# Kernel tuning notes

Hardware: AMD Instinct MI355X
Metric: run time of the kernel (lower is better)

The kernel has to match this reference:

```python
import jax, jax.numpy as jnp
import numpy as np

D_MODEL, D_STATE, D_CONV, EXPAND, HEADDIM, NGROUPS, CHUNK = 1024, 64, 4, 2, 64, 1, 64
D_INNER = EXPAND * D_MODEL          # 2048
NHEADS = D_INNER // HEADDIM         # 32
CONV_DIM = D_INNER + 2 * NGROUPS * D_STATE  # 2176
D_IN_PROJ = 2 * D_INNER + 2 * NGROUPS * D_STATE + NHEADS  # 4256
EPS = 1e-5


def segsum(x):
    """x: (..., T) -> (..., T, T) with out[i,j]=sum_{j<k<=i} x[k], -inf above diag."""
    T = x.shape[-1]
    i = jnp.arange(T)[:, None]
    j = jnp.arange(T)[None, :]
    xr = jnp.where(i > j, x[..., :, None], 0.0)   # keep x[...,i] at (i,j) when i>j
    s = jnp.cumsum(xr, axis=-2)
    return jnp.where(i >= j, s, -jnp.inf)


def setup_inputs() -> dict:
    key = jax.random.key(0)
    ks = jax.random.split(key, 10)
    B, L = 4, 4096
    u = jax.random.normal(ks[0], (B, L, D_MODEL), dtype=jnp.float32)
    in_proj_w = jax.random.normal(ks[1], (D_IN_PROJ, D_MODEL), dtype=jnp.float32) * (D_MODEL ** -0.5)
    conv_w = jax.random.normal(ks[2], (CONV_DIM, D_CONV), dtype=jnp.float32) * (D_CONV ** -0.5)
    conv_b = jax.random.normal(ks[3], (CONV_DIM,), dtype=jnp.float32) * 0.02
    init_states = jax.random.normal(ks[4], (NHEADS, HEADDIM, D_STATE), dtype=jnp.float32) * 0.02
    # dt_bias = inv softplus of dt sampled log-uniform in [1e-3, 1e-1]
    dt = jnp.exp(jax.random.uniform(ks[5], (NHEADS,)) * (np.log(0.1) - np.log(0.001)) + np.log(0.001))
    dt = jnp.clip(dt, 1e-4, None)
    dt_bias = dt + jnp.log(-jnp.expm1(-dt))
    A_log = jnp.log(jax.random.uniform(ks[6], (NHEADS,), minval=1.0, maxval=16.0))
    D = jnp.ones((NHEADS,), dtype=jnp.float32)
    norm_w = jnp.ones((D_INNER,), dtype=jnp.float32)
    out_proj_w = jax.random.normal(ks[7], (D_MODEL, D_INNER), dtype=jnp.float32) * (D_INNER ** -0.5)
    return {"u": u, "in_proj_w": in_proj_w, "conv_w": conv_w, "conv_b": conv_b,
            "init_states": init_states, "dt_bias": dt_bias, "A_log": A_log, "D": D,
            "norm_w": norm_w, "out_proj_w": out_proj_w}


def _forward(u, in_proj_w, conv_w, conv_b, init_states, dt_bias, A_log, D, norm_w, out_proj_w):
    b, L, _ = u.shape
    zxbcdt = jnp.einsum('bld,ed->ble', u, in_proj_w)
    z = zxbcdt[..., :D_INNER]
    xBC = zxbcdt[..., D_INNER:D_INNER + CONV_DIM]
    dt = jax.nn.softplus(zxbcdt[..., D_INNER + CONV_DIM:] + dt_bias)  # (b,L,h)
    # causal depthwise conv1d (padding=K-1, truncated to L) + SiLU
    xp = jnp.pad(xBC, ((0, 0), (D_CONV - 1, 0), (0, 0)))
    xBC = sum(xp[:, k:k + L, :] * conv_w[:, k] for k in range(D_CONV)) + conv_b
    xBC = jax.nn.silu(xBC)
    x = xBC[..., :D_INNER].reshape(b, L, NHEADS, HEADDIM)
    Bm = xBC[..., D_INNER:D_INNER + NGROUPS * D_STATE].reshape(b, L, NGROUPS, D_STATE)
    Cm = xBC[..., D_INNER + NGROUPS * D_STATE:].reshape(b, L, NGROUPS, D_STATE)
    A = -jnp.exp(A_log)  # (h,)
    # broadcast groups to heads (torch einsum broadcasts size-1 group dim)
    Bm = jnp.repeat(Bm, NHEADS // NGROUPS, axis=2)
    Cm = jnp.repeat(Cm, NHEADS // NGROUPS, axis=2)
    X = x * dt[..., None]          # (b,L,h,p)
    Adt = A * dt                   # (b,L,h)
    c = L // CHUNK
    Xc = X.reshape(b, c, CHUNK, NHEADS, HEADDIM)
    Bc = Bm.reshape(b, c, CHUNK, NHEADS, D_STATE)
    Cc = Cm.reshape(b, c, CHUNK, NHEADS, D_STATE)
    Ac = Adt.reshape(b, c, CHUNK, NHEADS).transpose(0, 3, 1, 2)  # (b,h,c,l)
    A_cumsum = jnp.cumsum(Ac, axis=-1)
    Lmat = jnp.exp(segsum(Ac))  # (b,h,c,l,l)
    Y_diag = jnp.einsum('bclhn,bcshn,bhcls,bcshp->bclhp', Cc, Bc, Lmat, Xc)
    decay_states = jnp.exp(A_cumsum[..., -1:] - A_cumsum)  # (b,h,c,l)
    states = jnp.einsum('bclhn,bhcl,bclhp->bchpn', Bc, decay_states, Xc)
    init = jnp.broadcast_to(init_states, (b,) + init_states.shape)[:, None]  # (b,1,h,p,n)
    states = jnp.concatenate([init, states], axis=1)  # (b,c+1,h,p,n)
    decay_chunk = jnp.exp(segsum(jnp.pad(A_cumsum[..., -1], ((0, 0), (0, 0), (1, 0)))))
    new_states = jnp.einsum('bhzc,bchpn->bzhpn', decay_chunk, states)
    states = new_states[:, :-1]
    state_decay_out = jnp.exp(A_cumsum)
    Y_off = jnp.einsum('bclhn,bchpn,bhcl->bclhp', Cc, states, state_decay_out)
    Y = (Y_diag + Y_off).reshape(b, L, NHEADS, HEADDIM) + x * D[:, None]
    y = Y.reshape(b, L, D_INNER)
    # gated RMSNorm (gate before norm)
    y = y * jax.nn.silu(z)
    y = y * jax.lax.rsqrt(jnp.mean(y * y, axis=-1, keepdims=True) + EPS) * norm_w
    return jnp.einsum('bld,ed->ble', y, out_proj_w)


def reference(u, in_proj_w, conv_w, conv_b, init_states, dt_bias, A_log, D, norm_w, out_proj_w):
    return _forward(u, in_proj_w, conv_w, conv_b, init_states, dt_bias, A_log, D, norm_w, out_proj_w)
```

## Files before the change

kernel.cpp:

```cpp
#include <hip/hip_runtime.h>
#include <math.h>

#define BATCH  4
#define LSEQ   4096
#define DMODEL 1024
#define DINNER 2048
#define NH     32
#define HD     64
#define DSTATE 64
#define CONVD  2176
#define NPROJ  4352
#define ZROW   4224
#define NCHUNK 64

typedef __attribute__((ext_vector_type(8))) short bf16x8;
typedef __attribute__((ext_vector_type(4))) float f32x4;

__device__ __forceinline__ float sigm(float x){ return 1.f/(1.f+expf(-x)); }

__device__ __forceinline__ unsigned short f2bf(float x){
    unsigned u = __float_as_uint(x);
    unsigned r = (u + 0x7fffu + ((u>>16)&1u)) >> 16;
    return (unsigned short)r;
}
__device__ __forceinline__ float bf2f(unsigned short h){
    return __uint_as_float(((unsigned)h)<<16);
}

__device__ __forceinline__ void gl2lds16(const unsigned short* g, short* l){
    __builtin_amdgcn_global_load_lds(
        (const __attribute__((address_space(1))) unsigned int*)g,
        (__attribute__((address_space(3))) unsigned int*)l, 16, 0, 0);
}

__global__ __launch_bounds__(256)
void f32_to_bf16(const float* __restrict__ in, unsigned short* __restrict__ o, size_t n)
{
    size_t i = ((size_t)blockIdx.x*256 + threadIdx.x)*8;
    if (i >= n) return;
    float4 a = *(const float4*)(in + i);
    float4 b = *(const float4*)(in + i + 4);
    uint4 v;
    v.x = (unsigned)f2bf(a.x) | ((unsigned)f2bf(a.y)<<16);
    v.y = (unsigned)f2bf(a.z) | ((unsigned)f2bf(a.w)<<16);
    v.z = (unsigned)f2bf(b.x) | ((unsigned)f2bf(b.y)<<16);
    v.w = (unsigned)f2bf(b.z) | ((unsigned)f2bf(b.w)<<16);
    *(uint4*)(o + i) = v;
}

template<int EPI>
__global__ __launch_bounds__(256)
void gemm_mfma(const unsigned short* __restrict__ A,
               const unsigned short* __restrict__ B,
               int K, int lda, int ldc, int ntiles, int Mrows,
               float* __restrict__ Cf,
               unsigned short* __restrict__ zxbc,
               float* __restrict__ dtout,
               const float* __restrict__ dt_bias,
               unsigned short* __restrict__ halo)
{
    __shared__ short As[128*32];
    __shared__ short Bs[128*32];
    const int tid  = threadIdx.x;
    const int wave = tid >> 6;
    const int lane = tid & 63;

    const int GM  = 16;
    const int pid = blockIdx.x;
    const int gsz = GM * ntiles;
    const int grp = pid / gsz;
    const int rem = pid - grp*gsz;
    const int bm  = (grp*GM + (rem & (GM-1))) * 128;
    const int bn  = (rem / GM) * 128;

    const int wr = (wave >> 1) * 64;
    const int wc = (wave & 1) * 64;
    const int quad = lane >> 4;
    const int l15  = lane & 15;

    f32x4 acc[4][4];
    #pragma unroll
    for (int i=0;i<4;i++)
        #pragma unroll
        for (int j=0;j<4;j++)
            acc[i][j] = (f32x4){0.f,0.f,0.f,0.f};

    const int srow = (lane >> 2);
    const int skc  = (lane & 3) * 8;

    for (int k0 = 0; k0 < K; k0 += 32){
        #pragma unroll
        for (int s=0; s<4; s++){
            int t = wave*4 + s;
            int r = (t & 7)*16 + srow;
            if (t < 8)
                gl2lds16(A + (size_t)(bm + r)*lda + k0 + skc, &As[(t & 7)*512]);
            else
                gl2lds16(B + (size_t)(bn + r)*K + k0 + skc, &Bs[(t & 7)*512]);
        }
        __syncthreads();
        bf16x8 af[4], bg[4];
        #pragma unroll
        for (int i=0;i<4;i++)
            af[i] = *(const bf16x8*)&As[(wr + i*16 + l15)*32 + quad*8];
        #pragma unroll
        for (int j=0;j<4;j++)
            bg[j] = *(const bf16x8*)&Bs[(wc + j*16 + l15)*32 + quad*8];
        #pragma unroll
        for (int i=0;i<4;i++)
            #pragma unroll
            for (int j=0;j<4;j++)
                acc[i][j] = __builtin_amdgcn_mfma_f32_16x16x32_bf16(af[i], bg[j], acc[i][j], 0,0,0);
        __syncthreads();
    }

    if (EPI == 0){
        #pragma unroll
        for (int i=0;i<4;i++)
            #pragma unroll
            for (int j=0;j<4;j++){
                int col = bn + wc + j*16 + l15;
                #pragma unroll
                for (int r=0;r<4;r++){
                    int row = bm + wr + i*16 + quad*4 + r;
                    Cf[(size_t)row*ldc + col] = acc[i][j][r];
                }
            }
    } else {
        if (bn < DINNER){
            #pragma unroll
            for (int i=0;i<4;i++)
                #pragma unroll
                for (int r=0;r<4;r++){
                    int row = bm + wr + i*16 + quad*4 + r;
                    #pragma unroll
                    for (int j=0;j<4;j++){
                        int col = bn + wc + j*16 + l15;
                        zxbc[(size_t)row*ZROW + col] = f2bf(acc[i][j][r]);
                    }
                }
        } else if (bn < DINNER + CONVD){
            #pragma unroll
            for (int i=0;i<4;i++)
                #pragma unroll
                for (int r=0;r<4;r++){
                    int row = bm + wr + i*16 + quad*4 + r;
                    int rel = row & 63;
                    int seg = (row >> 6) + 1;
                    #pragma unroll
                    for (int j=0;j<4;j++){
                        int col = bn + wc + j*16 + l15;
                        unsigned short v = f2bf(acc[i][j][r]);
                        zxbc[(size_t)row*ZROW + col] = v;
                        if (rel >= 61 && seg*64 < Mrows)
                            halo[((size_t)(seg*3 + (rel-61)))*CONVD + (col - DINNER)] = v;
                    }
                }
        } else if (wc == 0){
            #pragma unroll
            for (int j=0;j<2;j++){
                int h = j*16 + l15;
                #pragma unroll
                for (int i=0;i<4;i++)
                    #pragma unroll
                    for (int r=0;r<4;r++){
                        int row = bm + wr + i*16 + quad*4 + r;
                        float t = acc[i][j][r] + dt_bias[h];
                        dtout[(size_t)row*NH + h] = (t > 20.f) ? t : log1pf(expf(t));
                    }
            }
        }
    }
}

__global__ __launch_bounds__(256)
void conv_inplace(unsigned short* __restrict__ zxbc,
                  const unsigned short* __restrict__ halo,
                  const float* __restrict__ conv_w, const float* __restrict__ conv_b)
{
    int c = blockIdx.x*256 + threadIdx.x;
    if (c >= CONVD) return;
    int seg = blockIdx.y;
    const float w0=conv_w[c*4+0], w1=conv_w[c*4+1], w2=conv_w[c*4+2], w3=conv_w[c*4+3];
    const float bias = conv_b[c];
    float x0=0.f, x1=0.f, x2=0.f;
    if ((seg & 63) != 0){
        const unsigned short* hp = halo + (size_t)(seg*3)*CONVD + c;
        x0 = bf2f(hp[0]); x1 = bf2f(hp[CONVD]); x2 = bf2f(hp[2*CONVD]);
    }
    unsigned short* p = zxbc + (size_t)(seg*64)*ZROW + DINNER + c;
    for (int i=0;i<64;i++){
        float x3 = bf2f(*p);
        float v = fmaf(w0,x0,fmaf(w1,x1,fmaf(w2,x2,fmaf(w3,x3,bias))));
        *p = f2bf(v * sigm(v));
        x0=x1; x1=x2; x2=x3; p += ZROW;
    }
}

__global__ __launch_bounds__(256)
void states_intra(const unsigned short* __restrict__ zxbc,
                  const float* __restrict__ dtbuf,
                  const float* __restrict__ A_log,
                  unsigned short* __restrict__ locst,
                  float* __restrict__ acsbuf,
                  float* __restrict__ csumbuf)
{
    const int h = blockIdx.x, c = blockIdx.y;
    __shared__ unsigned short XT[64*72];
    __shared__ unsigned short BT[64*72];
    __shared__ float dt_sh[64], acs_sh[64], w_sh[64];
    const int tid = threadIdx.x;
    const size_t row0 = (size_t)(c*64)*ZROW;

    if (tid < 64) dt_sh[tid] = dtbuf[(size_t)(c*64+tid)*NH + h];
    __syncthreads();
    if (tid == 0){
        float Ah = -expf(A_log[h]); float s = 0.f;
        for (int l=0;l<64;l++){ s = fmaf(Ah, dt_sh[l], s); acs_sh[l] = s; }
    }
    __syncthreads();
    const float a63 = acs_sh[63];
    if (tid < 64){
        float a = acs_sh[tid];
        acsbuf[((size_t)c*NH + h)*64 + tid] = a;
        w_sh[tid] = expf(a63 - a) * dt_sh[tid];
    }
    if (tid == 0) csumbuf[(size_t)c*NH + h] = a63;
    __syncthreads();

    {
        const int l  = tid >> 2;
        const int f4 = tid & 3;
        const unsigned short* xr = zxbc + row0 + (size_t)l*ZROW;
        const float w = w_sh[l];
        #pragma unroll
        for (int q=0;q<4;q++){
            int col = f4*4 + q*16;
            uint2 xv = *(const uint2*)(xr + DINNER + h*HD + col);
            uint2 bv = *(const uint2*)(xr + DINNER + DINNER + col);
            XT[(col+0)*72 + l] = (unsigned short)(xv.x & 0xffff);
            XT[(col+1)*72 + l] = (unsigned short)(xv.x >> 16);
            XT[(col+2)*72 + l] = (unsigned short)(xv.y & 0xffff);
            XT[(col+3)*72 + l] = (unsigned short)(xv.y >> 16);
            BT[(col+0)*72 + l] = f2bf(bf2f((unsigned short)(bv.x & 0xffff))*w);
            BT[(col+1)*72 + l] = f2bf(bf2f((unsigned short)(bv.x >> 16))*w);
            BT[(col+2)*72 + l] = f2bf(bf2f((unsigned short)(bv.y & 0xffff))*w);
            BT[(col+3)*72 + l] = f2bf(bf2f((unsigned short)(bv.y >> 16))*w);
        }
    }
    __syncthreads();

    const int wave = tid >> 6, lane = tid & 63;
    const int quad = lane >> 4, l15 = lane & 15;
    f32x4 acc[4];
    #pragma unroll
    for (int j=0;j<4;j++) acc[j] = (f32x4){0.f,0.f,0.f,0.f};
    #pragma unroll
    for (int ks=0;ks<2;ks++){
        bf16x8 af = *(const bf16x8*)&XT[(wave*16 + l15)*72 + ks*32 + quad*8];
        #pragma unroll
        for (int j=0;j<4;j++){
            bf16x8 bf = *(const bf16x8*)&BT[(j*16 + l15)*72 + ks*32 + quad*8];
            acc[j] = __builtin_amdgcn_mfma_f32_16x16x32_bf16(af, bf, acc[j], 0,0,0);
        }
    }
    const size_t sbase = ((size_t)c*NH + h)*4096;
    #pragma unroll
    for (int j=0;j<4;j++)
        #pragma unroll
        for (int r=0;r<4;r++){
            int p = wave*16 + quad*4 + r;
            int n = j*16 + l15;
            locst[sbase + (size_t)p*64 + n] = f2bf(acc[j][r]);
        }
}

__global__ __launch_bounds__(256)
void chunk_scan(unsigned short* __restrict__ states,
                const float* __restrict__ csumbuf,
                const float* __restrict__ init_states)
{
    const int h = blockIdx.x, half = blockIdx.y, b = blockIdx.z;
    __shared__ float cs_sh[64];
    const int tid = threadIdx.x;
    if (tid < 64) cs_sh[tid] = csumbuf[(size_t)(b*64 + tid)*NH + h];
    __syncthreads();
    const int e0 = half*2048 + tid*8;
    float S[8];
    {
        const float4* ip = (const float4*)(init_states + (size_t)h*4096 + e0);
        float4 v0 = ip[0], v1 = ip[1];
        S[0]=v0.x; S[1]=v0.y; S[2]=v0.z; S[3]=v0.w;
        S[4]=v1.x; S[5]=v1.y; S[6]=v1.z; S[7]=v1.w;
    }
    for (int zg=0; zg<8; zg++){
        uint4 L[8];
        #pragma unroll
        for (int k=0;k<8;k++)
            L[k] = *(const uint4*)(states + ((size_t)(b*64 + zg*8+k)*NH + h)*4096 + e0);
        #pragma unroll
        for (int k=0;k<8;k++){
            int z = zg*8 + k;
            float dec = expf(cs_sh[z]);
            uint4 o;
            o.x = (unsigned)f2bf(S[0]) | ((unsigned)f2bf(S[1])<<16);
            o.y = (unsigned)f2bf(S[2]) | ((unsigned)f2bf(S[3])<<16);
            o.z = (unsigned)f2bf(S[4]) | ((unsigned)f2bf(S[5])<<16);
            o.w = (unsigned)f2bf(S[6]) | ((unsigned)f2bf(S[7])<<16);
            *(uint4*)(states + ((size_t)(b*64 + z)*NH + h)*4096 + e0) = o;
            unsigned a[4] = {L[k].x, L[k].y, L[k].z, L[k].w};
            #pragma unroll
            for (int q=0;q<4;q++){
                float lo = bf2f((unsigned short)(a[q]&0xffff));
                float hi = bf2f((unsigned short)(a[q]>>16));
                S[q*2+0] = fmaf(dec, S[q*2+0], lo);
                S[q*2+1] = fmaf(dec, S[q*2+1], hi);
            }
        }
    }
}

__global__ __launch_bounds__(256)
void y_fused(unsigned short* __restrict__ zxbc,
             const float* __restrict__ dtbuf,
             const unsigned short* __restrict__ entst,
             const float* __restrict__ acsbuf,
             const float* __restrict__ Dvec)
{
    const int h = blockIdx.x, c = blockIdx.y;
    __shared__ unsigned short Cr[64*72];
    __shared__ unsigned short Ce[64*72];
    __shared__ unsigned short Bm[64*72];
    __shared__ unsigned short XT[64*72];
    __shared__ unsigned short Sv[64*72];
    __shared__ float acs_sh[64], dt_sh[64], ea_sh[64];
    const int tid = threadIdx.x;
    const size_t row0 = (size_t)(c*64)*ZROW;
    const size_t sbase = ((size_t)c*NH + h)*4096;

    if (tid < 64){
        float a = acsbuf[((size_t)c*NH + h)*64 + tid];
        acs_sh[tid] = a;
        ea_sh[tid]  = expf(a);
        dt_sh[tid]  = dtbuf[(size_t)(c*64 + tid)*NH + h];
    }
    __syncthreads();

    {
        const int l  = tid >> 2;
        const int f4 = tid & 3;
        const unsigned short* xr = zxbc + row0 + (size_t)l*ZROW;
        const float el = ea_sh[l];
        #pragma unroll
        for (int q=0;q<4;q++){
            int col = f4*4 + q*16;
            uint2 cv = *(const uint2*)(xr + DINNER + DINNER + DSTATE + col);
            uint2 bv = *(const uint2*)(xr + DINNER + DINNER + col);
            uint2 xv = *(const uint2*)(xr + DINNER + h*HD + col);
            *(uint2*)&Cr[l*72 + col] = cv;
            *(uint2*)&Bm[l*72 + col] = bv;
            unsigned short* ce = &Ce[l*72 + col];
            ce[0] = f2bf(bf2f((unsigned short)(cv.x & 0xffff))*el);
            ce[1] = f2bf(bf2f((unsigned short)(cv.x >> 16))*el);
            ce[2] = f2bf(bf2f((unsigned short)(cv.y & 0xffff))*el);
            ce[3] = f2bf(bf2f((unsigned short)(cv.y >> 16))*el);
            XT[(col+0)*72 + l] = (unsigned short)(xv.x & 0xffff);
            XT[(col+1)*72 + l] = (unsigned short)(xv.x >> 16);
            XT[(col+2)*72 + l] = (unsigned short)(xv.y & 0xffff);
            XT[(col+3)*72 + l] = (unsigned short)(xv.y >> 16);
            *(uint2*)&Sv[l*72 + col] = *(const uint2*)(entst + sbase + (size_t)l*64 + col);
        }
    }
    __syncthreads();

    const int wave = tid >> 6, lane = tid & 63;
    const int quad = lane >> 4, l15 = lane & 15;

    f32x4 g[4];
    #pragma unroll
    for (int j=0;j<4;j++) g[j] = (f32x4){0.f,0.f,0.f,0.f};
    #pragma unroll
    for (int ks=0;ks<2;ks++){
        bf16x8 af = *(const bf16x8*)&Cr[(wave*16 + l15)*72 + ks*32 + quad*8];
        #pragma unroll
        for (int j=0;j<4;j++){
            bf16x8 bf = *(const bf16x8*)&Bm[(j*16 + l15)*72 + ks*32 + quad*8];
            g[j] = __builtin_amdgcn_mfma_f32_16x16x32_bf16(af, bf, g[j], 0,0,0);
        }
    }
    __syncthreads();

    const float Dh = Dvec[h];
    #pragma unroll
    for (int j=0;j<4;j++)
        #pragma unroll
        for (int r=0;r<4;r++){
            int l = wave*16 + quad*4 + r;
            int s = j*16 + l15;
            float v = (s <= l) ? g[j][r]*expf(acs_sh[l]-acs_sh[s])*dt_sh[s] : 0.f;
            if (s == l) v += Dh;
            Bm[l*72 + s] = f2bf(v);
        }
    __syncthreads();

    f32x4 y[4];
    #pragma unroll
    for (int j=0;j<4;j++) y[j] = (f32x4){0.f,0.f,0.f,0.f};
    #pragma unroll
    for (int ks=0;ks<2;ks++){
        bf16x8 a1 = *(const bf16x8*)&Bm[(wave*16 + l15)*72 + ks*32 + quad*8];
        bf16x8 a2 = *(const bf16x8*)&Ce[(wave*16 + l15)*72 + ks*32 + quad*8];
        #pragma unroll
        for (int j=0;j<4;j++){
            bf16x8 b1 = *(const bf16x8*)&XT[(j*16 + l15)*72 + ks*32 + quad*8];
            bf16x8 b2 = *(const bf16x8*)&Sv[(j*16 + l15)*72 + ks*32 + quad*8];
            y[j] = __builtin_amdgcn_mfma_f32_16x16x32_bf16(a1, b1, y[j], 0,0,0);
            y[j] = __builtin_amdgcn_mfma_f32_16x16x32_bf16(a2, b2, y[j], 0,0,0);
        }
    }

    #pragma unroll
    for (int j=0;j<4;j++)
        #pragma unroll
        for (int r=0;r<4;r++){
            int l = wave*16 + quad*4 + r;
            int p = j*16 + l15;
            zxbc[row0 + (size_t)l*ZROW + DINNER + h*HD + p] = f2bf(y[j][r]);
        }
}

__global__ __launch_bounds__(256)
void gate_norm(unsigned short* __restrict__ zxbc, const float* __restrict__ norm_w)
{
    const int m = blockIdx.x;
    const int tid = threadIdx.x;
    unsigned short* row = zxbc + (size_t)m*ZROW;
    uint4 zv = *(const uint4*)(row + tid*8);
    uint4 yv = *(const uint4*)(row + DINNER + tid*8);
    unsigned zz[4] = {zv.x, zv.y, zv.z, zv.w};
    unsigned yy[4] = {yv.x, yv.y, yv.z, yv.w};
    float g[8];
    float acc = 0.f;
    #pragma unroll
    for (int q=0;q<4;q++){
        float zl = bf2f((unsigned short)(zz[q]&0xffff));
        float zh = bf2f((unsigned short)(zz[q]>>16));
        float yl = bf2f((unsigned short)(yy[q]&0xffff));
        float yh = bf2f((unsigned short)(yy[q]>>16));
        g[q*2+0] = yl * zl * sigm(zl);
        g[q*2+1] = yh * zh * sigm(zh);
        acc += g[q*2]*g[q*2] + g[q*2+1]*g[q*2+1];
    }
    #pragma unroll
    for (int o=32;o>0;o>>=1) acc += __shfl_down(acc, o, 64);
    __shared__ float red[4];
    if ((tid & 63)==0) red[tid>>6] = acc;
    __syncthreads();
    float tot = red[0]+red[1]+red[2]+red[3];
    float scale = rsqrtf(tot * (1.f/2048.f) + 1e-5f);
    const float* nw = norm_w + tid*8;
    float4 w0 = *(const float4*)nw;
    float4 w1 = *(const float4*)(nw+4);
    float Wv[8] = {w0.x,w0.y,w0.z,w0.w,w1.x,w1.y,w1.z,w1.w};
    uint4 ov;
    unsigned ow[4];
    #pragma unroll
    for (int q=0;q<4;q++){
        unsigned short lo = f2bf(g[q*2+0]*scale*Wv[q*2+0]);
        unsigned short hi = f2bf(g[q*2+1]*scale*Wv[q*2+1]);
        ow[q] = (unsigned)lo | ((unsigned)hi<<16);
    }
    ov.x=ow[0]; ov.y=ow[1]; ov.z=ow[2]; ov.w=ow[3];
    *(uint4*)(row + tid*8) = ov;
}

extern "C" void kernel_launch(void* const* d_in, const int* in_sizes, int n_in,
                              void* d_out, int out_size, void* d_ws, size_t ws_size,
                              hipStream_t stream) {
    const float* u           = (const float*)d_in[0];
    const float* in_proj_w   = (const float*)d_in[1];
    const float* conv_w      = (const float*)d_in[2];
    const float* conv_b      = (const float*)d_in[3];
    const float* init_states = (const float*)d_in[4];
    const float* dt_bias     = (const float*)d_in[5];
    const float* A_log       = (const float*)d_in[6];
    const float* Dv          = (const float*)d_in[7];
    const float* norm_w      = (const float*)d_in[8];
    const float* out_proj_w  = (const float*)d_in[9];
    float* out = (float*)d_out;
    char* wsb = (char*)d_ws;

    const size_t BIG_BYTES = 226197504;
    const bool big = (ws_size >= BIG_BYTES);
    const int nb = big ? BATCH : 1;
    const size_t Mrows = (size_t)nb * LSEQ;

    size_t off = 0;
    unsigned short* zxbc    = (unsigned short*)(wsb + off); off += Mrows*ZROW*2;
    unsigned short* statesz = (unsigned short*)(wsb + off);
    unsigned short* ubf     = statesz;
    off += Mrows/64 * NH*HD*DSTATE*2;
    unsigned short* wibf    = (unsigned short*)(wsb + off); off += (size_t)NPROJ*DMODEL*2;
    unsigned short* woutbf  = (unsigned short*)(wsb + off); off += (size_t)DMODEL*DINNER*2;
    float*          dtbuf   = (float*)(wsb + off);   off += Mrows*NH*4;
    float*          acsbuf  = (float*)(wsb + off);   off += Mrows/64 * NH*64*4;
    float*          csumbuf = (float*)(wsb + off);   off += Mrows/64 * NH*4;
    unsigned short* halo    = (unsigned short*)(wsb + off); off += Mrows/64 * 3*CONVD*2;

    f32_to_bf16<<<dim3((4256*1024/8 + 255)/256), 256, 0, stream>>>(
        in_proj_w, wibf, (size_t)4256*1024);
    f32_to_bf16<<<dim3(1024*2048/8/256), 256, 0, stream>>>(
        out_proj_w, woutbf, (size_t)1024*2048);

    const int npass = big ? 1 : BATCH;
    for (int b=0; b<npass; b++){
        const float* ub   = u   + (size_t)b*LSEQ*DMODEL;
        float*       outb = out + (size_t)b*LSEQ*DMODEL;
        const int mt = (int)(Mrows/128);

        f32_to_bf16<<<dim3(Mrows*DMODEL/8/256), 256, 0, stream>>>(
            ub, ubf, Mrows*DMODEL);
        gemm_mfma<1><<<dim3((NPROJ/128) * mt), 256, 0, stream>>>(
            ubf, wibf, DMODEL, DMODEL, 0, NPROJ/128, (int)Mrows,
            nullptr, zxbc, dtbuf, dt_bias, halo);
        conv_inplace<<<dim3(9, (unsigned)(Mrows/64)), 256, 0, stream>>>(
            zxbc, halo, conv_w, conv_b);
        states_intra<<<dim3(NH, (unsigned)(Mrows/64)), 256, 0, stream>>>(
            zxbc, dtbuf, A_log, statesz, acsbuf, csumbuf);
        chunk_scan<<<dim3(NH, 2, nb), 256, 0, stream>>>(
            statesz, csumbuf, init_states);
        y_fused<<<dim3(NH, (unsigned)(Mrows/64)), 256, 0, stream>>>(
            zxbc, dtbuf, statesz, acsbuf, Dv);
        gate_norm<<<dim3((unsigned)Mrows), 256, 0, stream>>>(zxbc, norm_w);
        gemm_mfma<0><<<dim3((DMODEL/128) * mt), 256, 0, stream>>>(
            zxbc, woutbf, DINNER, ZROW, DMODEL, DMODEL/128, (int)Mrows,
            outb, nullptr, nullptr, nullptr, nullptr);
    }
}
```

Baseline: 646.0 us.

## Replace 128x128 GEMM with 256x256 multi-buffered pipelined MFMA kernel

Both projection GEMMs move to a new 512-thread kernel with 256x256 tiles. It keeps a 4-stage LDS ring buffer filled by direct global-to-LDS loads that are prefetched three k-steps ahead, and uses an XOR-swizzled LDS layout. MFMA bursts are split into two halves, each bracketed by s_setprio and explicit waitcnt/barrier control, and workgroups are remapped with an XCD-aware interleave. The aim is to hide memory latency and raise arithmetic intensity per tile. In exchange it uses far more LDS and registers (lower occupancy), and the 256-wide N tiles make the in-proj epilogue branch per 16-column sub-block.

```diff
diff --git a/kernel.cpp b/kernel.cpp
--- a/kernel.cpp
+++ b/kernel.cpp
@@ -33,6 +33,12 @@
         (__attribute__((address_space(3))) unsigned int*)l, 16, 0, 0);
 }
 
+__device__ __forceinline__ void wg_bar(){
+    asm volatile("" ::: "memory");
+    __builtin_amdgcn_s_barrier();
+    asm volatile("" ::: "memory");
+}
+
 __global__ __launch_bounds__(256)
 void f32_to_bf16(const float* __restrict__ in, unsigned short* __restrict__ o, size_t n)
 {
@@ -48,128 +54,147 @@
     *(uint4*)(o + i) = v;
 }
 
+__device__ __forceinline__ void stage_tile(const unsigned short* __restrict__ G,
+                                           int ld, int b0, int kt,
+                                           short* sl, int wid, int lane)
+{
+    const int r  = lane >> 2;
+    const int sc = (((lane & 3) ^ ((lane >> 3) & 3)) << 3);
+    #pragma unroll
+    for (int c=0;c<2;c++){
+        int row = wid*32 + c*16 + r;
+        gl2lds16(G + (size_t)(b0 + row)*ld + kt*32 + sc,
+                 sl + wid*1024 + c*512);
+    }
+}
+
 template<int EPI>
-__global__ __launch_bounds__(256)
-void gemm_mfma(const unsigned short* __restrict__ A,
-               const unsigned short* __restrict__ B,
-               int K, int lda, int ldc, int ntiles, int Mrows,
-               float* __restrict__ Cf,
-               unsigned short* __restrict__ zxbc,
-               float* __restrict__ dtout,
-               const float* __restrict__ dt_bias,
-               unsigned short* __restrict__ halo)
-{
-    __shared__ short As[128*32];
-    __shared__ short Bs[128*32];
+__global__ __launch_bounds__(512)
+void gemm256(const unsigned short* __restrict__ A,
+             const unsigned short* __restrict__ B,
+             int K, int lda, int ldb, int ldc, int MT, int NT, int Mrows,
+             float* __restrict__ Cf,
+             unsigned short* __restrict__ zxbc,
+             float* __restrict__ dtout,
+             const float* __restrict__ dt_bias,
+             unsigned short* __restrict__ halo)
+{
+    __shared__ short As[4][256*32];
+    __shared__ short Bs[4][256*32];
     const int tid  = threadIdx.x;
-    const int wave = tid >> 6;
+    const int wid  = tid >> 6;
     const int lane = tid & 63;
-
-    const int GM  = 16;
-    const int pid = blockIdx.x;
-    const int gsz = GM * ntiles;
-    const int grp = pid / gsz;
-    const int rem = pid - grp*gsz;
-    const int bm  = (grp*GM + (rem & (GM-1))) * 128;
-    const int bn  = (rem / GM) * 128;
-
-    const int wr = (wave >> 1) * 64;
-    const int wc = (wave & 1) * 64;
-    const int quad = lane >> 4;
-    const int l15  = lane & 15;
-
-    f32x4 acc[4][4];
-    #pragma unroll
-    for (int i=0;i<4;i++)
-        #pragma unroll
-        for (int j=0;j<4;j++)
-            acc[i][j] = (f32x4){0.f,0.f,0.f,0.f};
-
-    const int srow = (lane >> 2);
-    const int skc  = (lane & 3) * 8;
-
-    for (int k0 = 0; k0 < K; k0 += 32){
-        #pragma unroll
-        for (int s=0; s<4; s++){
-            int t = wave*4 + s;
-            int r = (t & 7)*16 + srow;
-            if (t < 8)
-                gl2lds16(A + (size_t)(bm + r)*lda + k0 + skc, &As[(t & 7)*512]);
-            else
-                gl2lds16(B + (size_t)(bn + r)*K + k0 + skc, &Bs[(t & 7)*512]);
-        }
-        __syncthreads();
+    const int widm = wid >> 2, widn = wid & 3;
+    const int quad = lane >> 4, l15 = lane & 15;
+
+    const int nwg = MT * NT;
+    const int per = nwg >> 3;
+    const int logical = (blockIdx.x & 7) * per + (blockIdx.x >> 3);
+    const int bm = (logical % MT) * 256;
+    const int bn = (logical / MT) * 256;
+
+    const int nkt = K >> 5;
+
+    const int aoff = l15*32 + ((quad ^ ((l15>>1)&3)) << 3);
+
+    f32x4 acc[8][4];
+    #pragma unroll
+    for (int i=0;i<8;i++)
+        #pragma unroll
+        for (int j=0;j<4;j++) acc[i][j] = (f32x4){0.f,0.f,0.f,0.f};
+
+    #pragma unroll
+    for (int t=0;t<3;t++){
+        stage_tile(A, lda, bm, t, &As[t][0], wid, lane);
+        stage_tile(B, ldb, bn, t, &Bs[t][0], wid, lane);
+    }
+    asm volatile("s_waitcnt vmcnt(8)" ::: "memory");
+    wg_bar();
+
+    for (int kt=0; kt<nkt; ++kt){
+        const short* Asl = &As[kt&3][0];
+        const short* Bsl = &Bs[kt&3][0];
         bf16x8 af[4], bg[4];
         #pragma unroll
-        for (int i=0;i<4;i++)
-            af[i] = *(const bf16x8*)&As[(wr + i*16 + l15)*32 + quad*8];
-        #pragma unroll
-        for (int j=0;j<4;j++)
-            bg[j] = *(const bf16x8*)&Bs[(wc + j*16 + l15)*32 + quad*8];
-        #pragma unroll
-        for (int i=0;i<4;i++)
+        for (int mi=0;mi<4;mi++)
+            af[mi] = *(const bf16x8*)(Asl + widm*4096 + mi*512 + aoff);
+        #pragma unroll
+        for (int ni=0;ni<4;ni++)
+            bg[ni] = *(const bf16x8*)(Bsl + widn*2048 + ni*512 + aoff);
+        if (kt+3 < nkt)
+            stage_tile(A, lda, bm, kt+3, &As[(kt+3)&3][0], wid, lane);
+        wg_bar();
+        asm volatile("s_waitcnt lgkmcnt(0)" ::: "memory");
+        __builtin_amdgcn_s_setprio(1);
+        #pragma unroll
+        for (int mi=0;mi<4;mi++)
             #pragma unroll
-            for (int j=0;j<4;j++)
-                acc[i][j] = __builtin_amdgcn_mfma_f32_16x16x32_bf16(af[i], bg[j], acc[i][j], 0,0,0);
-        __syncthreads();
+            for (int ni=0;ni<4;ni++)
+                acc[mi][ni] = __builtin_amdgcn_mfma_f32_16x16x32_bf16(af[mi], bg[ni], acc[mi][ni], 0,0,0);
+        __builtin_amdgcn_s_setprio(0);
+        wg_bar();
+        #pragma unroll
+        for (int mi=0;mi<4;mi++)
+            af[mi] = *(const bf16x8*)(Asl + widm*4096 + (mi+4)*512 + aoff);
+        if (kt+3 < nkt)
+            stage_tile(B, ldb, bn, kt+3, &Bs[(kt+3)&3][0], wid, lane);
+        {
+            int d = nkt - 2 - kt;
+            if (d >= 2)      asm volatile("s_waitcnt vmcnt(8)" ::: "memory");
+            else if (d == 1) asm volatile("s_waitcnt vmcnt(4)" ::: "memory");
+            else if (d == 0) asm volatile("s_waitcnt vmcnt(0)" ::: "memory");
+        }
+        wg_bar();
+        asm volatile("s_waitcnt lgkmcnt(0)" ::: "memory");
+        __builtin_amdgcn_s_setprio(1);
+        #pragma unroll
+        for (int mi=0;mi<4;mi++)
+            #pragma unroll
+            for (int ni=0;ni<4;ni++)
+                acc[mi+4][ni] = __builtin_amdgcn_mfma_f32_16x16x32_bf16(af[mi], bg[ni], acc[mi+4][ni], 0,0,0);
+        __builtin_amdgcn_s_setprio(0);
+        wg_bar();
     }
 
     if (EPI == 0){
         #pragma unroll
-        for (int i=0;i<4;i++)
+        for (int mi=0;mi<8;mi++)
             #pragma unroll
-            for (int j=0;j<4;j++){
-                int col = bn + wc + j*16 + l15;
+            for (int r=0;r<4;r++){
+                int row = bm + widm*128 + mi*16 + quad*4 + r;
                 #pragma unroll
-                for (int r=0;r<4;r++){
-                    int row = bm + wr + i*16 + quad*4 + r;
-                    Cf[(size_t)row*ldc + col] = acc[i][j][r];
+                for (int ni=0;ni<4;ni++){
+                    int col = bn + widn*64 + ni*16 + l15;
+                    Cf[(size_t)row*ldc + col] = acc[mi][ni][r];
                 }
             }
     } else {
-        if (bn < DINNER){
+        #pragma unroll
+        for (int mi=0;mi<8;mi++)
             #pragma unroll
-            for (int i=0;i<4;i++)
+            for (int r=0;r<4;r++){
+                int row = bm + widm*128 + mi*16 + quad*4 + r;
+                int rel = row & 63;
+                int seg = (row >> 6) + 1;
                 #pragma unroll
-                for (int r=0;r<4;r++){
-                    int row = bm + wr + i*16 + quad*4 + r;
-                    #pragma unroll
-                    for (int j=0;j<4;j++){
-                        int col = bn + wc + j*16 + l15;
-                        zxbc[(size_t)row*ZROW + col] = f2bf(acc[i][j][r]);
+                for (int ni=0;ni<4;ni++){
+                    int cb  = bn + widn*64 + ni*16;
+                    int col = cb + l15;
+                    float v = acc[mi][ni][r];
+                    if (cb < DINNER){
+                        zxbc[(size_t)row*ZROW + col] = f2bf(v);
+                    } else if (cb < DINNER + CONVD){
+                        unsigned short q = f2bf(v);
+                        zxbc[(size_t)row*ZROW + col] = q;
+                        if (rel >= 61 && seg*64 < Mrows)
+                            halo[((size_t)(seg*3 + (rel-61)))*CONVD + (col - DINNER)] = q;
+                    } else if (cb < DINNER + CONVD + NH){
+                        int h = col - (DINNER + CONVD);
+                        float t = v + dt_bias[h];
+                        dtout[(size_t)row*NH + h] = (t > 20.f) ? t : log1pf(expf(t));
                     }
                 }
-        } else if (bn < DINNER + CONVD){
-            #pragma unroll
-            for (int i=0;i<4;i++)
-                #pragma unroll
-                for (int r=0;r<4;r++){
-                    int row = bm + wr + i*16 + quad*4 + r;
-                    int rel = row & 63;
-                    int seg = (row >> 6) + 1;
-                    #pragma unroll
-                    for (int j=0;j<4;j++){
-                        int col = bn + wc + j*16 + l15;
-                        unsigned short v = f2bf(acc[i][j][r]);
-                        zxbc[(size_t)row*ZROW + col] = v;
-                        if (rel >= 61 && seg*64 < Mrows)
-                            halo[((size_t)(seg*3 + (rel-61)))*CONVD + (col - DINNER)] = v;
-                    }
-                }
-        } else if (wc == 0){
-            #pragma unroll
-            for (int j=0;j<2;j++){
-                int h = j*16 + l15;
-                #pragma unroll
-                for (int i=0;i<4;i++)
-                    #pragma unroll
-                    for (int r=0;r<4;r++){
-                        int row = bm + wr + i*16 + quad*4 + r;
-                        float t = acc[i][j][r] + dt_bias[h];
-                        dtout[(size_t)row*NH + h] = (t > 20.f) ? t : log1pf(expf(t));
-                    }
             }
-        }
     }
 }
 
@@ -516,12 +541,12 @@
     for (int b=0; b<npass; b++){
         const float* ub   = u   + (size_t)b*LSEQ*DMODEL;
         float*       outb = out + (size_t)b*LSEQ*DMODEL;
-        const int mt = (int)(Mrows/128);
+        const int MT = (int)(Mrows/256);
 
         f32_to_bf16<<<dim3(Mrows*DMODEL/8/256), 256, 0, stream>>>(
             ub, ubf, Mrows*DMODEL);
-        gemm_mfma<1><<<dim3((NPROJ/128) * mt), 256, 0, stream>>>(
-            ubf, wibf, DMODEL, DMODEL, 0, NPROJ/128, (int)Mrows,
+        gemm256<1><<<dim3(MT * (NPROJ/256)), 512, 0, stream>>>(
+            ubf, wibf, DMODEL, DMODEL, DMODEL, 0, MT, NPROJ/256, (int)Mrows,
             nullptr, zxbc, dtbuf, dt_bias, halo);
         conv_inplace<<<dim3(9, (unsigned)(Mrows/64)), 256, 0, stream>>>(
             zxbc, halo, conv_w, conv_b);
@@ -532,8 +557,8 @@
         y_fused<<<dim3(NH, (unsigned)(Mrows/64)), 256, 0, stream>>>(
             zxbc, dtbuf, statesz, acsbuf, Dv);
         gate_norm<<<dim3((unsigned)Mrows), 256, 0, stream>>>(zxbc, norm_w);
-        gemm_mfma<0><<<dim3((DMODEL/128) * mt), 256, 0, stream>>>(
-            zxbc, woutbf, DINNER, ZROW, DMODEL, DMODEL/128, (int)Mrows,
+        gemm256<0><<<dim3(MT * (DMODEL/256)), 512, 0, stream>>>(
+            zxbc, woutbf, DINNER, ZROW, DINNER, DMODEL, MT, DMODEL/256, (int)Mrows,
             outb, nullptr, nullptr, nullptr, nullptr);
     }
 }
```

Result: slower. 704.6 us (+9.1%).
